# Kernel optimization log

Hardware: AMD Instinct MI355X
Metric: run time of the kernel (lower is better)

## Reference

```python
import jax, jax.numpy as jnp
import numpy as np

HIDDEN = 4096
HEADS = 64
HEAD_DIM = HIDDEN // HEADS  # 64
ROT = int(HEAD_DIM * 0.5)   # 32 rotary dims (partial rotary)
THETA = 25000.0
EPS = 1e-5
B, S = 1, 2048


def setup_inputs() -> dict:
    key = jax.random.key(0)
    ks = jax.random.split(key, 8)
    hidden_states = jax.random.normal(ks[0], (B, S, HIDDEN), dtype=jnp.float32)
    # additive causal mask: 0 on/below diagonal, -inf above
    causal = jnp.triu(jnp.full((S, S), -1e9, dtype=jnp.float32), k=1)
    attention_mask = causal[None, None, :, :]
    position_ids = jnp.arange(S, dtype=jnp.int64 if jax.config.jax_enable_x64 else jnp.int32)[None, :]
    sc = 0.02
    W_qkv = jax.random.normal(ks[1], (3 * HIDDEN, HIDDEN), dtype=jnp.float32) * sc
    b_qkv = jnp.zeros((3 * HIDDEN,), dtype=jnp.float32)
    q_ln_w = jnp.ones((HEAD_DIM,), dtype=jnp.float32)
    q_ln_b = jnp.zeros((HEAD_DIM,), dtype=jnp.float32)
    k_ln_w = jnp.ones((HEAD_DIM,), dtype=jnp.float32)
    k_ln_b = jnp.zeros((HEAD_DIM,), dtype=jnp.float32)
    W_dense = jax.random.normal(ks[2], (HIDDEN, HIDDEN), dtype=jnp.float32) * sc
    b_dense = jnp.zeros((HIDDEN,), dtype=jnp.float32)
    return dict(hidden_states=hidden_states, attention_mask=attention_mask,
                W_qkv=W_qkv, b_qkv=b_qkv, q_ln_w=q_ln_w, q_ln_b=q_ln_b,
                k_ln_w=k_ln_w, k_ln_b=k_ln_b, W_dense=W_dense, b_dense=b_dense,
                position_ids=position_ids)


def _layernorm(x, w, b):
    mu = jnp.mean(x, axis=-1, keepdims=True)
    var = jnp.var(x, axis=-1, keepdims=True)
    return (x - mu) * jax.lax.rsqrt(var + EPS) * w + b


def _rotate_half(x):
    h = x.shape[-1] // 2
    return jnp.concatenate((-x[..., h:], x[..., :h]), axis=-1)


def reference(hidden_states, attention_mask, W_qkv, b_qkv, q_ln_w, q_ln_b,
              k_ln_w, k_ln_b, W_dense, b_dense, position_ids):
    b, s, _ = hidden_states.shape
    # fused QKV projection, split interleaved per head: [b,s,H,3,d]
    fused = hidden_states @ W_qkv.T + b_qkv
    fused = fused.reshape(b, s, HEADS, 3, HEAD_DIM)
    q, k, v = fused[..., 0, :], fused[..., 1, :], fused[..., 2, :]
    # per-head QK LayerNorm (over head_dim)
    q = _layernorm(q, q_ln_w, q_ln_b)
    k = _layernorm(k, k_ln_w, k_ln_b)
    # [b,H,s,d]
    q = q.transpose(0, 2, 1, 3)
    k = k.transpose(0, 2, 1, 3)
    v = v.transpose(0, 2, 1, 3)
    # rotary embeddings (default rope, scaling 1.0)
    inv_freq = 1.0 / (THETA ** (jnp.arange(0, ROT, 2, dtype=jnp.float32) / ROT))
    freqs = position_ids.astype(jnp.float32)[:, :, None] * inv_freq[None, None, :]  # [b,s,ROT/2]
    emb = jnp.concatenate((freqs, freqs), axis=-1)  # [b,s,ROT]
    cos = jnp.cos(emb)[:, None, :, :].astype(hidden_states.dtype)  # [b,1,s,ROT]
    sin = jnp.sin(emb)[:, None, :, :].astype(hidden_states.dtype)
    # partial rotary: rotate first ROT dims, pass-through the rest
    q_rot, q_pass = q[..., :ROT], q[..., ROT:]
    k_rot, k_pass = k[..., :ROT], k[..., ROT:]
    q_rot = q_rot * cos + _rotate_half(q_rot) * sin
    k_rot = k_rot * cos + _rotate_half(k_rot) * sin
    q = jnp.concatenate((q_rot, q_pass), axis=-1)
    k = jnp.concatenate((k_rot, k_pass), axis=-1)
    # causal attention
    scores = jnp.einsum('bhqd,bhkd->bhqk', q, k) / np.sqrt(HEAD_DIM).astype(np.float32)
    scores = scores + attention_mask
    probs = jax.nn.softmax(scores.astype(jnp.float32), axis=-1).astype(q.dtype)
    attn = jnp.einsum('bhqk,bhkd->bhqd', probs, v)
    attn = attn.transpose(0, 2, 1, 3).reshape(b, s, HIDDEN)
    return attn @ W_dense.T + b_dense
```

## Files before the change

kernel.cpp:

```cpp
#include <hip/hip_runtime.h>
#include <hip/hip_bf16.h>


using short8 = __attribute__((ext_vector_type(8))) short;
using f32x4  = __attribute__((ext_vector_type(4))) float;

#define HIDDEN 4096
#define HEADS  64
#define HD     64
#define SLEN   2048
#define QSCALE 0.18033688011112042f

__device__ inline float bf2f(__hip_bfloat16 v) { return __bfloat162float(v); }
__device__ inline __hip_bfloat16 f2bf(float f) { return __float2bfloat16(f); }
__device__ inline unsigned short f2bfbits(float f) {
    return __builtin_bit_cast(unsigned short, __float2bfloat16(f));
}
__device__ inline short8 pack8(float4 a, float4 b) {
    short8 r;
    r[0] = (short)f2bfbits(a.x); r[1] = (short)f2bfbits(a.y);
    r[2] = (short)f2bfbits(a.z); r[3] = (short)f2bfbits(a.w);
    r[4] = (short)f2bfbits(b.x); r[5] = (short)f2bfbits(b.y);
    r[6] = (short)f2bfbits(b.z); r[7] = (short)f2bfbits(b.w);
    return r;
}
__device__ inline int pk2(float lo, float hi) {
    return (int)(((unsigned)f2bfbits(hi) << 16) | (unsigned)f2bfbits(lo));
}

__device__ inline void load_lds16(const void* g, void* l) {
    __builtin_amdgcn_global_load_lds(
        (const __attribute__((address_space(1))) void*)g,
        (__attribute__((address_space(3))) void*)l, 16, 0, 0);
}

__global__ __launch_bounds__(256)
void cvt_f32_bf16(const float* __restrict__ in, __hip_bfloat16* __restrict__ out, int n8)
{
    const int stride = gridDim.x * blockDim.x;
    for (int i = blockIdx.x * blockDim.x + threadIdx.x; i < n8; i += stride) {
        const float4 a = *(const float4*)(in + (size_t)i * 8);
        const float4 b = *(const float4*)(in + (size_t)i * 8 + 4);
        *(short8*)(out + (size_t)i * 8) = pack8(a, b);
    }
}

__global__ __launch_bounds__(512, 2)
void gemm_qkv(const __hip_bfloat16* __restrict__ A, const __hip_bfloat16* __restrict__ B,
              const float* __restrict__ bias,
              __hip_bfloat16* __restrict__ q0, __hip_bfloat16* __restrict__ o1,
              __hip_bfloat16* __restrict__ o2, int M, int N, int K)
{
    __shared__ __align__(16) __hip_bfloat16 Abuf[2][16384];
    __shared__ __align__(16) __hip_bfloat16 Bbuf[2][12288];

    const int tid  = threadIdx.x;
    const int wid  = tid >> 6;
    const int lane = tid & 63;
    const int lr   = lane & 15;
    const int lg   = lane >> 4;

    const int nwg = gridDim.x * gridDim.y;
    int flat = blockIdx.y * gridDim.x + blockIdx.x;
    flat = (flat & 7) * (nwg >> 3) + (flat >> 3);
    const int bm = (flat % gridDim.x) * 256;
    const int bn = (flat / gridDim.x) * 192;

    const int wr = (wid >> 2) * 128;
    const int wc = (wid & 3) * 48;

    const int scol = 8 * ((lane & 7) ^ ((lane >> 3) & 7));
    const __hip_bfloat16* PA = A + (size_t)(bm + wid * 32 + (lane >> 3)) * K + scol;
    const __hip_bfloat16* PB = B + (size_t)(bn + wid * 24 + (lane >> 3)) * K + scol;
    const int ldA = wid * 2048;
    const int ldB = wid * 1536;

#define SH_A(tile, buf) { \
    const __hip_bfloat16* g_ = PA + (size_t)(tile) * 64; \
    load_lds16(g_,                  &Abuf[buf][ldA]); \
    load_lds16(g_ + (size_t)8 * K,  &Abuf[buf][ldA + 512]); \
    load_lds16(g_ + (size_t)16 * K, &Abuf[buf][ldA + 1024]); \
    load_lds16(g_ + (size_t)24 * K, &Abuf[buf][ldA + 1536]); }
#define SH_B(tile, buf) { \
    const __hip_bfloat16* g_ = PB + (size_t)(tile) * 64; \
    load_lds16(g_,                  &Bbuf[buf][ldB]); \
    load_lds16(g_ + (size_t)8 * K,  &Bbuf[buf][ldB + 512]); \
    load_lds16(g_ + (size_t)16 * K, &Bbuf[buf][ldB + 1024]); }

    const int slot = lg ^ (lr & 7);
    const char* A0k0 = (const char*)&Abuf[0][0] + (wr + lr) * 128 + slot * 16;
    const char* A0k1 = (const char*)&Abuf[0][0] + (wr + lr) * 128 + (slot ^ 4) * 16;
    const char* A1k0 = (const char*)&Abuf[1][0] + (wr + lr) * 128 + slot * 16;
    const char* A1k1 = (const char*)&Abuf[1][0] + (wr + lr) * 128 + (slot ^ 4) * 16;
    const char* B0k0 = (const char*)&Bbuf[0][0] + (wc + lr) * 128 + slot * 16;
    const char* B0k1 = (const char*)&Bbuf[0][0] + (wc + lr) * 128 + (slot ^ 4) * 16;
    const char* B1k0 = (const char*)&Bbuf[1][0] + (wc + lr) * 128 + slot * 16;
    const char* B1k1 = (const char*)&Bbuf[1][0] + (wc + lr) * 128 + (slot ^ 4) * 16;

    f32x4 acc[8][3] = {};
    short8 af[4][2], bfL[2][2], bfH[1][2];

#define RD_AF(K0, K1, MOFF) { \
    _Pragma("unroll") \
    for (int mm = 0; mm < 4; ++mm) { \
        af[mm][0] = *(const short8*)((K0) + ((MOFF) + mm) * 2048); \
        af[mm][1] = *(const short8*)((K1) + ((MOFF) + mm) * 2048); } }
#define RD_BL(K0, K1) { \
    _Pragma("unroll") \
    for (int nn = 0; nn < 2; ++nn) { \
        bfL[nn][0] = *(const short8*)((K0) + nn * 2048); \
        bfL[nn][1] = *(const short8*)((K1) + nn * 2048); } }
#define RD_BH(K0, K1) { \
    bfH[0][0] = *(const short8*)((K0) + 2 * 2048); \
    bfH[0][1] = *(const short8*)((K1) + 2 * 2048); }
#define MFMA_BLK2(MB) \
    __builtin_amdgcn_s_setprio(1); \
    { _Pragma("unroll") \
      for (int mm = 0; mm < 4; ++mm) { \
        _Pragma("unroll") \
        for (int nn = 0; nn < 2; ++nn) { \
            acc[(MB) + mm][nn] = __builtin_amdgcn_mfma_f32_16x16x32_bf16(af[mm][0], bfL[nn][0], acc[(MB) + mm][nn], 0, 0, 0); \
            acc[(MB) + mm][nn] = __builtin_amdgcn_mfma_f32_16x16x32_bf16(af[mm][1], bfL[nn][1], acc[(MB) + mm][nn], 0, 0, 0); } } } \
    __builtin_amdgcn_s_setprio(0);
#define MFMA_BLK1(MB) \
    __builtin_amdgcn_s_setprio(1); \
    { _Pragma("unroll") \
      for (int mm = 0; mm < 4; ++mm) { \
        acc[(MB) + mm][2] = __builtin_amdgcn_mfma_f32_16x16x32_bf16(af[mm][0], bfH[0][0], acc[(MB) + mm][2], 0, 0, 0); \
        acc[(MB) + mm][2] = __builtin_amdgcn_mfma_f32_16x16x32_bf16(af[mm][1], bfH[0][1], acc[(MB) + mm][2], 0, 0, 0); } } \
    __builtin_amdgcn_s_setprio(0);

    SH_A(0, 0); SH_B(0, 0);
    SH_A(1, 1); SH_B(1, 1);
    asm volatile("s_waitcnt vmcnt(7)\n\ts_barrier" ::: "memory");

    const int nt2 = K >> 7;
    #pragma unroll 1
    for (int j = 0; j < nt2; ++j) {
        const bool st = (j < nt2 - 1);
        const int t2 = 2 * j + 2, t3 = 2 * j + 3;

        RD_AF(A0k0, A0k1, 0); RD_BL(B0k0, B0k1);
        __builtin_amdgcn_s_barrier();
        MFMA_BLK2(0);
        __builtin_amdgcn_s_barrier();

        RD_BH(B0k0, B0k1);
        __builtin_amdgcn_s_barrier();
        MFMA_BLK1(0);
        __builtin_amdgcn_s_barrier();

        RD_AF(A0k0, A0k1, 4);
        if (st) SH_B(t2, 0);
        __builtin_amdgcn_s_barrier();
        MFMA_BLK2(4);
        __builtin_amdgcn_s_barrier();

        if (st) SH_A(t2, 0);
        __builtin_amdgcn_s_barrier();
        MFMA_BLK1(4);
        if (st) asm volatile("s_waitcnt vmcnt(7)\n\ts_barrier" ::: "memory");
        else    asm volatile("s_waitcnt vmcnt(0)\n\ts_barrier" ::: "memory");

        RD_AF(A1k0, A1k1, 0); RD_BL(B1k0, B1k1);
        __builtin_amdgcn_s_barrier();
        MFMA_BLK2(0);
        __builtin_amdgcn_s_barrier();

        RD_BH(B1k0, B1k1);
        __builtin_amdgcn_s_barrier();
        MFMA_BLK1(0);
        __builtin_amdgcn_s_barrier();

        RD_AF(A1k0, A1k1, 4);
        if (st) SH_B(t3, 1);
        __builtin_amdgcn_s_barrier();
        MFMA_BLK2(4);
        __builtin_amdgcn_s_barrier();

        if (st) SH_A(t3, 1);
        __builtin_amdgcn_s_barrier();
        MFMA_BLK1(4);
        if (st) asm volatile("s_waitcnt vmcnt(7)\n\ts_barrier" ::: "memory");
    }
#undef SH_A
#undef SH_B
#undef RD_AF
#undef RD_BL
#undef RD_BH
#undef MFMA_BLK2
#undef MFMA_BLK1

    #pragma unroll
    for (int n = 0; n < 3; ++n) {
        const int cb    = bn + wc + n * 16;
        const int c64   = cb >> 6;
        const int which = c64 % 3;
        const int h     = c64 / 3;
        const int d     = (cb & 63) + lr;
        const float bb  = bias[cb + lr];

        if (which == 2) {
            #pragma unroll
            for (int m = 0; m < 8; ++m) {
                const int row = bm + wr + m * 16 + lg * 4;
                int2 w;
                w.x = pk2(acc[m][n][0] + bb, acc[m][n][1] + bb);
                w.y = pk2(acc[m][n][2] + bb, acc[m][n][3] + bb);
                *(int2*)(o2 + ((size_t)(h * HD + d)) * SLEN + row) = w;
            }
        } else {
            __hip_bfloat16* outp = (which == 0) ? q0 : o1;
            #pragma unroll
            for (int m = 0; m < 8; ++m)
                #pragma unroll
                for (int e = 0; e < 4; ++e) {
                    const int row = bm + wr + m * 16 + lg * 4 + e;
                    outp[(size_t)row * HIDDEN + h * HD + d] = f2bf(acc[m][n][e] + bb);
                }
        }
    }
}

__global__ __launch_bounds__(256, 4)
void gemm_d(const __hip_bfloat16* __restrict__ A, const __hip_bfloat16* __restrict__ B,
            const float* __restrict__ bias, float* __restrict__ C, int M, int N, int K)
{
    __shared__ __align__(16) __hip_bfloat16 Abuf[2][128 * 32];
    __shared__ __align__(16) __hip_bfloat16 Bbuf[2][128 * 32];

    const int tid  = threadIdx.x;
    const int wid  = tid >> 6;
    const int lane = tid & 63;
    const int lr   = lane & 15;
    const int lg   = lane >> 4;

    const int nwg = gridDim.x * gridDim.y;
    int flat = blockIdx.y * gridDim.x + blockIdx.x;
    flat = (flat & 7) * (nwg >> 3) + (flat >> 3);
    const int bm = (flat % gridDim.x) * 128;
    const int bn = (flat / gridDim.x) * 128;

    const int wr = (wid >> 1) * 64;
    const int wc = (wid & 1) * 64;

    const int srow = lane >> 2;
    const int sc   = lane & 3;
    const int scol = (sc ^ ((srow >> 1) & 3)) * 8;
    const __hip_bfloat16* Ag = A + (size_t)(bm + wid * 16 + srow) * K + scol;
    const __hip_bfloat16* Bg = B + (size_t)(bn + wid * 16 + srow) * K + scol;
    const int ldsW = wid * 512;

    const int rswz = (lr >> 1) & 3;
    const int rdAoff = (wr + lr) * 64 + ((lg ^ rswz) * 16);
    const int rdBoff = (wc + lr) * 64 + ((lg ^ rswz) * 16);

    f32x4 acc[4][4] = {};
    const int nt = K >> 5;

#define STG_D(t, slot) { \
    const __hip_bfloat16* gA = Ag + (size_t)(t) * 32; \
    const __hip_bfloat16* gB = Bg + (size_t)(t) * 32; \
    load_lds16(gA,                  &Abuf[slot][ldsW]); \
    load_lds16(gA + (size_t)64 * K, &Abuf[slot][ldsW + 2048]); \
    load_lds16(gB,                  &Bbuf[slot][ldsW]); \
    load_lds16(gB + (size_t)64 * K, &Bbuf[slot][ldsW + 2048]); }

    STG_D(0, 0);
    asm volatile("s_waitcnt vmcnt(0)\n\ts_barrier" ::: "memory");

    #pragma unroll 1
    for (int t = 0; t < nt; ++t) {
        const int s = t & 1;
        const char* As = (const char*)&Abuf[s][0];
        const char* Bs = (const char*)&Bbuf[s][0];

        if (t + 1 < nt) STG_D(t + 1, s ^ 1);

        short8 af[4], bf[4];
        #pragma unroll
        for (int m = 0; m < 4; ++m)
            af[m] = *(const short8*)(As + rdAoff + m * 1024);
        #pragma unroll
        for (int n = 0; n < 4; ++n)
            bf[n] = *(const short8*)(Bs + rdBoff + n * 1024);

        __builtin_amdgcn_s_setprio(1);
        #pragma unroll
        for (int m = 0; m < 4; ++m)
            #pragma unroll
            for (int n = 0; n < 4; ++n)
                acc[m][n] = __builtin_amdgcn_mfma_f32_16x16x32_bf16(af[m], bf[n], acc[m][n], 0, 0, 0);
        __builtin_amdgcn_s_setprio(0);

        asm volatile("s_waitcnt vmcnt(0)\n\ts_barrier" ::: "memory");
    }
#undef STG_D

    #pragma unroll
    for (int m = 0; m < 4; ++m)
        #pragma unroll
        for (int n = 0; n < 4; ++n) {
            const int col = bn + wc + n * 16 + lr;
            const float bv = bias[col];
            #pragma unroll
            for (int e = 0; e < 4; ++e) {
                const int row = bm + wr + m * 16 + lg * 4 + e;
                C[(size_t)row * N + col] = acc[m][n][e] + bv;
            }
        }
}

template<int MODE, bool AF32, bool BF32>
__global__ __launch_bounds__(256)
void gemm_nt(const void* __restrict__ Ap, const void* __restrict__ Bp,
             const float* __restrict__ bias,
             void* __restrict__ o0, __hip_bfloat16* __restrict__ o1,
             __hip_bfloat16* __restrict__ o2, int M, int N, int K)
{
    __shared__ __align__(16) unsigned char AbufRaw[AF32 ? 16384 : 8192];
    __shared__ __align__(16) unsigned char BbufRaw[BF32 ? 16384 : 8192];
    const int tid  = threadIdx.x;
    const int wid  = tid >> 6;
    const int lane = tid & 63;
    const int bm   = blockIdx.x * 128;
    const int bn   = blockIdx.y * 128;
    const int wr   = (wid >> 1) * 64;
    const int wc   = (wid & 1) * 64;
    const int lr   = lane & 15;
    const int lg   = lane >> 4;

    f32x4 acc[4][4] = {};

    for (int k0 = 0; k0 < K; k0 += 32) {
        __syncthreads();
        if constexpr (AF32) {
            const float* Af = (const float*)Ap;
            const int r = lane >> 3, c4 = (lane & 7) * 4;
            #pragma unroll
            for (int i = 0; i < 4; ++i) {
                const int rb = i * 32 + wid * 8;
                load_lds16(Af + (size_t)(bm + rb + r) * K + k0 + c4, (float*)AbufRaw + rb * 32);
            }
        } else {
            const __hip_bfloat16* Ab16 = (const __hip_bfloat16*)Ap;
            const int sr2 = lane >> 2, sc = (lane & 3) * 8;
            #pragma unroll
            for (int i = 0; i < 2; ++i) {
                const int rb = (wid * 2 + i) * 16;
                load_lds16(Ab16 + (size_t)(bm + rb + sr2) * K + k0 + sc,
                           (__hip_bfloat16*)AbufRaw + rb * 32);
            }
        }
        if constexpr (BF32) {
            const float* Bf = (const float*)Bp;
            const int r = lane >> 3, c4 = (lane & 7) * 4;
            #pragma unroll
            for (int i = 0; i < 4; ++i) {
                const int rb = i * 32 + wid * 8;
                load_lds16(Bf + (size_t)(bn + rb + r) * K + k0 + c4, (float*)BbufRaw + rb * 32);
            }
        } else {
            const __hip_bfloat16* Bb16 = (const __hip_bfloat16*)Bp;
            const int sr2 = lane >> 2, sc = (lane & 3) * 8;
            #pragma unroll
            for (int i = 0; i < 2; ++i) {
                const int rb = (wid * 2 + i) * 16;
                load_lds16(Bb16 + (size_t)(bn + rb + sr2) * K + k0 + sc,
                           (__hip_bfloat16*)BbufRaw + rb * 32);
            }
        }
        __syncthreads();

        short8 af[4], bfr[4];
        #pragma unroll
        for (int m = 0; m < 4; ++m) {
            const int row = wr + m * 16 + lr;
            if constexpr (AF32) {
                const float* Ab = (const float*)AbufRaw;
                af[m] = pack8(*(const float4*)(Ab + row * 32 + lg * 8),
                              *(const float4*)(Ab + row * 32 + lg * 8 + 4));
            } else {
                af[m] = *(const short8*)((const __hip_bfloat16*)AbufRaw + row * 32 + lg * 8);
            }
        }
        #pragma unroll
        for (int n = 0; n < 4; ++n) {
            const int row = wc + n * 16 + lr;
            if constexpr (BF32) {
                const float* Bb = (const float*)BbufRaw;
                bfr[n] = pack8(*(const float4*)(Bb + row * 32 + lg * 8),
                               *(const float4*)(Bb + row * 32 + lg * 8 + 4));
            } else {
                bfr[n] = *(const short8*)((const __hip_bfloat16*)BbufRaw + row * 32 + lg * 8);
            }
        }
        #pragma unroll
        for (int m = 0; m < 4; ++m)
            #pragma unroll
            for (int n = 0; n < 4; ++n)
                acc[m][n] = __builtin_amdgcn_mfma_f32_16x16x32_bf16(af[m], bfr[n], acc[m][n], 0, 0, 0);
    }

    #pragma unroll
    for (int m = 0; m < 4; ++m) {
        #pragma unroll
        for (int n = 0; n < 4; ++n) {
            const int col = bn + wc + n * 16 + lr;
            const float bv = bias[col];
            #pragma unroll
            for (int e = 0; e < 4; ++e) {
                const int row = bm + wr + m * 16 + lg * 4 + e;
                const float v = acc[m][n][e] + bv;
                if (MODE == 0) {
                    ((float*)o0)[(size_t)row * N + col] = v;
                } else {
                    const int h     = col / 192;
                    const int rem   = col - h * 192;
                    const int which = rem >> 6;
                    const int d     = rem & 63;
                    __hip_bfloat16* q0p = (__hip_bfloat16*)o0;
                    if (which == 0)      q0p[(size_t)row * HIDDEN + h * HD + d] = f2bf(v);
                    else if (which == 1) o1[(size_t)row * HIDDEN + h * HD + d] = f2bf(v);
                    else                 o2[((size_t)(h * HD + d)) * SLEN + row] = f2bf(v);
                }
            }
        }
    }
}

__global__ __launch_bounds__(256)
void ln_rope(__hip_bfloat16* __restrict__ Qp,
             __hip_bfloat16* __restrict__ Kp,
             const float* __restrict__ qw, const float* __restrict__ qb,
             const float* __restrict__ kw, const float* __restrict__ kb)
{
    const int wi   = blockIdx.x * 4 + (threadIdx.x >> 6);
    const int lane = threadIdx.x & 63;
    const int s = wi >> 6;
    const int h = wi & 63;
    const int d = lane;

    const size_t idx = (size_t)s * HIDDEN + h * HD + d;
    float q = bf2f(Qp[idx]);
    float k = bf2f(Kp[idx]);

    float qs = q, ks = k;
    #pragma unroll
    for (int m = 1; m < 64; m <<= 1) { qs += __shfl_xor(qs, m); ks += __shfl_xor(ks, m); }
    const float qmean = qs * (1.0f / 64.0f), kmean = ks * (1.0f / 64.0f);
    const float qd = q - qmean, kd = k - kmean;
    float qv = qd * qd, kv = kd * kd;
    #pragma unroll
    for (int m = 1; m < 64; m <<= 1) { qv += __shfl_xor(qv, m); kv += __shfl_xor(kv, m); }
    const float qr = rsqrtf(qv * (1.0f / 64.0f) + 1e-5f);
    const float kr = rsqrtf(kv * (1.0f / 64.0f) + 1e-5f);
    float qn = qd * qr * qw[d] + qb[d];
    float kn = kd * kr * kw[d] + kb[d];

    const float qo = __shfl_xor(qn, 16);
    const float ko = __shfl_xor(kn, 16);
    if (d < 32) {
        const int   i   = d & 15;
        const float inv = expf(-0.6329144439906461f * (float)i);
        const float ang = (float)s * inv;
        const float c = cosf(ang), sn = sinf(ang);
        const float qrh = (d < 16) ? -qo : qo;
        const float krh = (d < 16) ? -ko : ko;
        qn = qn * c + qrh * sn;
        kn = kn * c + krh * sn;
    }
    qn *= QSCALE;

    Qp[idx] = f2bf(qn);
    Kp[idx] = f2bf(kn);
}

__global__ __launch_bounds__(256)
void flash_attn(const __hip_bfloat16* __restrict__ Q,
                const __hip_bfloat16* __restrict__ Kb,
                const __hip_bfloat16* __restrict__ Vt,
                __hip_bfloat16* __restrict__ Ao)
{
    const int wid  = threadIdx.x >> 6;
    const int lane = threadIdx.x & 63;
    int bidx = blockIdx.x;
    bidx = (bidx & 7) * 64 + (bidx >> 3);
    const int qg   = 31 - (bidx & 31);
    const int h    = (bidx >> 5) * 4 + wid;
    const int lr   = lane & 15;
    const int lg   = lane >> 4;
    const int src0 = lr + (((2 * lg) & 3) << 4);
    const int src1 = src0 + 16;

    const int qrowA = (4 * qg + 0) * 16 + lr;
    const int qrowB = (4 * qg + 1) * 16 + lr;
    const int qrowC = (4 * qg + 2) * 16 + lr;
    const int qrowD = (4 * qg + 3) * 16 + lr;

    const __hip_bfloat16* qbA = Q + (size_t)qrowA * HIDDEN + h * HD + lg * 8;
    const __hip_bfloat16* qbB = Q + (size_t)qrowB * HIDDEN + h * HD + lg * 8;
    const __hip_bfloat16* qbC = Q + (size_t)qrowC * HIDDEN + h * HD + lg * 8;
    const __hip_bfloat16* qbD = Q + (size_t)qrowD * HIDDEN + h * HD + lg * 8;
    const short8 qaA0 = *(const short8*)qbA;
    const short8 qaA1 = *(const short8*)(qbA + 32);
    const short8 qaB0 = *(const short8*)qbB;
    const short8 qaB1 = *(const short8*)(qbB + 32);
    const short8 qaC0 = *(const short8*)qbC;
    const short8 qaC1 = *(const short8*)(qbC + 32);
    const short8 qaD0 = *(const short8*)qbD;
    const short8 qaD1 = *(const short8*)(qbD + 32);

    f32x4 accA[4] = {}, accB[4] = {}, accC[4] = {}, accD[4] = {};
    float lpA = 0.0f, lpB = 0.0f, lpC = 0.0f, lpD = 0.0f;

    const int nt     = 2 * qg + 2;
    const int ftiles = 2 * qg;

    const __hip_bfloat16* kp = Kb + (size_t)lr * HIDDEN + h * HD + lg * 8;
    short8 k00 = *(const short8*)kp;
    short8 k01 = *(const short8*)(kp + 32);
    short8 k10 = *(const short8*)(kp + (size_t)16 * HIDDEN);
    short8 k11 = *(const short8*)(kp + (size_t)16 * HIDDEN + 32);

#define SM_PV(MASKED, S0, S1, QROW, LP, ACC) { \
    float p0[4], p1[4]; \
    _Pragma("unroll") \
    for (int e = 0; e < 4; ++e) { \
        if (MASKED) { \
            const int krow = kv0 + lg * 4 + e; \
            p0[e] = (krow      <= (QROW)) ? exp2f(S0[e]) : 0.0f; \
            p1[e] = (krow + 16 <= (QROW)) ? exp2f(S1[e]) : 0.0f; \
        } else { \
            p0[e] = exp2f(S0[e]); \
            p1[e] = exp2f(S1[e]); \
        } \
        LP += p0[e] + p1[e]; \
    } \
    const int a0 = pk2(p0[0], p0[1]), a1 = pk2(p0[2], p0[3]); \
    const int b0 = pk2(p1[0], p1[1]), b1 = pk2(p1[2], p1[3]); \
    const int za00 = __shfl(a0, src0), za10 = __shfl(a1, src0); \
    const int za01 = __shfl(a0, src1), za11 = __shfl(a1, src1); \
    const int zb00 = __shfl(b0, src0), zb10 = __shfl(b1, src0); \
    const int zb01 = __shfl(b0, src1), zb11 = __shfl(b1, src1); \
    int4 W; \
    W.x = (lg < 2) ? za00 : zb00; \
    W.y = (lg < 2) ? za10 : zb10; \
    W.z = (lg < 2) ? za01 : zb01; \
    W.w = (lg < 2) ? za11 : zb11; \
    const short8 pB_ = __builtin_bit_cast(short8, W); \
    _Pragma("unroll") \
    for (int n = 0; n < 4; ++n) \
        ACC[n] = __builtin_amdgcn_mfma_f32_16x16x32_bf16(vf[n], pB_, ACC[n], 0, 0, 0); }

#define FA_TILE(MASKED) { \
    const int kv0 = t * 32; \
    short8 vf[4]; \
    _Pragma("unroll") \
    for (int n = 0; n < 4; ++n) \
        vf[n] = *(const short8*)(Vt + ((size_t)(h * HD + n * 16 + lr)) * SLEN + kv0 + lg * 8); \
    f32x4 sA0 = {-8.f, -8.f, -8.f, -8.f}; \
    f32x4 sA1 = {-8.f, -8.f, -8.f, -8.f}; \
    f32x4 sB0 = {-8.f, -8.f, -8.f, -8.f}; \
    f32x4 sB1 = {-8.f, -8.f, -8.f, -8.f}; \
    f32x4 sC0 = {-8.f, -8.f, -8.f, -8.f}; \
    f32x4 sC1 = {-8.f, -8.f, -8.f, -8.f}; \
    f32x4 sD0 = {-8.f, -8.f, -8.f, -8.f}; \
    f32x4 sD1 = {-8.f, -8.f, -8.f, -8.f}; \
    sA0 = __builtin_amdgcn_mfma_f32_16x16x32_bf16(k00, qaA0, sA0, 0, 0, 0); \
    sB0 = __builtin_amdgcn_mfma_f32_16x16x32_bf16(k00, qaB0, sB0, 0, 0, 0); \
    sC0 = __builtin_amdgcn_mfma_f32_16x16x32_bf16(k00, qaC0, sC0, 0, 0, 0); \
    sD0 = __builtin_amdgcn_mfma_f32_16x16x32_bf16(k00, qaD0, sD0, 0, 0, 0); \
    sA0 = __builtin_amdgcn_mfma_f32_16x16x32_bf16(k01, qaA1, sA0, 0, 0, 0); \
    sB0 = __builtin_amdgcn_mfma_f32_16x16x32_bf16(k01, qaB1, sB0, 0, 0, 0); \
    sC0 = __builtin_amdgcn_mfma_f32_16x16x32_bf16(k01, qaC1, sC0, 0, 0, 0); \
    sD0 = __builtin_amdgcn_mfma_f32_16x16x32_bf16(k01, qaD1, sD0, 0, 0, 0); \
    sA1 = __builtin_amdgcn_mfma_f32_16x16x32_bf16(k10, qaA0, sA1, 0, 0, 0); \
    sB1 = __builtin_amdgcn_mfma_f32_16x16x32_bf16(k10, qaB0, sB1, 0, 0, 0); \
    sC1 = __builtin_amdgcn_mfma_f32_16x16x32_bf16(k10, qaC0, sC1, 0, 0, 0); \
    sD1 = __builtin_amdgcn_mfma_f32_16x16x32_bf16(k10, qaD0, sD1, 0, 0, 0); \
    sA1 = __builtin_amdgcn_mfma_f32_16x16x32_bf16(k11, qaA1, sA1, 0, 0, 0); \
    sB1 = __builtin_amdgcn_mfma_f32_16x16x32_bf16(k11, qaB1, sB1, 0, 0, 0); \
    sC1 = __builtin_amdgcn_mfma_f32_16x16x32_bf16(k11, qaC1, sC1, 0, 0, 0); \
    sD1 = __builtin_amdgcn_mfma_f32_16x16x32_bf16(k11, qaD1, sD1, 0, 0, 0); \
    short8 n00, n01, n10, n11; \
    if (t + 1 < nt) { \
        const __hip_bfloat16* np = kp + (size_t)(kv0 + 32) * HIDDEN; \
        n00 = *(const short8*)np; \
        n01 = *(const short8*)(np + 32); \
        n10 = *(const short8*)(np + (size_t)16 * HIDDEN); \
        n11 = *(const short8*)(np + (size_t)16 * HIDDEN + 32); \
    } \
    SM_PV(MASKED, sA0, sA1, qrowA, lpA, accA) \
    SM_PV(MASKED, sB0, sB1, qrowB, lpB, accB) \
    SM_PV(MASKED, sC0, sC1, qrowC, lpC, accC) \
    SM_PV(MASKED, sD0, sD1, qrowD, lpD, accD) \
    k00 = n00; k01 = n01; k10 = n10; k11 = n11; }

    int t = 0;
    #pragma unroll 1
    for (; t < ftiles; ++t) FA_TILE(false)
    #pragma unroll 1
    for (; t < nt; ++t) FA_TILE(true)
#undef FA_TILE
#undef SM_PV

#define FIN(LP, INV) \
    { float lr_ = LP; lr_ += __shfl_xor(lr_, 16); lr_ += __shfl_xor(lr_, 32); INV = 1.0f / lr_; }
    float invA, invB, invC, invD;
    FIN(lpA, invA) FIN(lpB, invB) FIN(lpC, invC) FIN(lpD, invD)
#undef FIN

    __hip_bfloat16* opA = Ao + (size_t)qrowA * HIDDEN + h * HD + lg * 4;
    __hip_bfloat16* opB = Ao + (size_t)qrowB * HIDDEN + h * HD + lg * 4;
    __hip_bfloat16* opC = Ao + (size_t)qrowC * HIDDEN + h * HD + lg * 4;
    __hip_bfloat16* opD = Ao + (size_t)qrowD * HIDDEN + h * HD + lg * 4;
    #pragma unroll
    for (int n = 0; n < 4; ++n) {
        int2 w;
        w.x = pk2(accA[n][0] * invA, accA[n][1] * invA);
        w.y = pk2(accA[n][2] * invA, accA[n][3] * invA);
        *(int2*)(opA + n * 16) = w;
        w.x = pk2(accB[n][0] * invB, accB[n][1] * invB);
        w.y = pk2(accB[n][2] * invB, accB[n][3] * invB);
        *(int2*)(opB + n * 16) = w;
        w.x = pk2(accC[n][0] * invC, accC[n][1] * invC);
        w.y = pk2(accC[n][2] * invC, accC[n][3] * invC);
        *(int2*)(opC + n * 16) = w;
        w.x = pk2(accD[n][0] * invD, accD[n][1] * invD);
        w.y = pk2(accD[n][2] * invD, accD[n][3] * invD);
        *(int2*)(opD + n * 16) = w;
    }
}

extern "C" void kernel_launch(void* const* d_in, const int* in_sizes, int n_in,
                              void* d_out, int out_size, void* d_ws, size_t ws_size,
                              hipStream_t stream)
{
    const float* hidden = (const float*)d_in[0];
    const float* Wqkv = (const float*)d_in[2];
    const float* bqkv = (const float*)d_in[3];
    const float* qlw  = (const float*)d_in[4];
    const float* qlb  = (const float*)d_in[5];
    const float* klw  = (const float*)d_in[6];
    const float* klb  = (const float*)d_in[7];
    const float* Wd   = (const float*)d_in[8];
    const float* bd   = (const float*)d_in[9];

    char* ws = (char*)d_ws;
    const size_t SEG = (size_t)SLEN * HIDDEN * sizeof(__hip_bfloat16);
    if (ws_size < 4 * SEG) return;
    __hip_bfloat16* Qpre = (__hip_bfloat16*)(ws + 0 * SEG);
    __hip_bfloat16* Kpre = (__hip_bfloat16*)(ws + 1 * SEG);
    __hip_bfloat16* Vt   = (__hip_bfloat16*)(ws + 2 * SEG);
    __hip_bfloat16* Ao   = (__hip_bfloat16*)(ws + 3 * SEG);

    const bool fast = (ws_size >= 13 * SEG);

    if (fast) {
        __hip_bfloat16* hid16  = (__hip_bfloat16*)(ws + 4 * SEG);
        __hip_bfloat16* Wqkv16 = (__hip_bfloat16*)(ws + 5 * SEG);
        __hip_bfloat16* Wd16   = (__hip_bfloat16*)(ws + 11 * SEG);

        cvt_f32_bf16<<<2048, 256, 0, stream>>>(hidden, hid16,  SLEN * HIDDEN / 8);
        cvt_f32_bf16<<<2048, 256, 0, stream>>>(Wqkv,   Wqkv16, 3 * HIDDEN * HIDDEN / 8);
        cvt_f32_bf16<<<2048, 256, 0, stream>>>(Wd,     Wd16,   HIDDEN * HIDDEN / 8);

        gemm_qkv<<<dim3(8, 64), 512, 0, stream>>>(
            hid16, Wqkv16, bqkv, Qpre, Kpre, Vt, SLEN, 3 * HIDDEN, HIDDEN);
        ln_rope<<<dim3(SLEN * HEADS / 4), 256, 0, stream>>>(Qpre, Kpre, qlw, qlb, klw, klb);
        flash_attn<<<dim3((HEADS / 4) * 32), 256, 0, stream>>>(Qpre, Kpre, Vt, Ao);
        gemm_d<<<dim3(16, 32), 256, 0, stream>>>(
            Ao, Wd16, bd, (float*)d_out, SLEN, HIDDEN, HIDDEN);
    } else {
        gemm_nt<1, true, true><<<dim3(16, 96), 256, 0, stream>>>(
            hidden, Wqkv, bqkv, Qpre, Kpre, Vt, SLEN, 3 * HIDDEN, HIDDEN);
        ln_rope<<<dim3(SLEN * HEADS / 4), 256, 0, stream>>>(Qpre, Kpre, qlw, qlb, klw, klb);
        flash_attn<<<dim3((HEADS / 4) * 32), 256, 0, stream>>>(Qpre, Kpre, Vt, Ao);
        gemm_nt<0, false, true><<<dim3(16, 32), 256, 0, stream>>>(
            Ao, Wd, bd, d_out, nullptr, nullptr, SLEN, HIDDEN, HIDDEN);
    }
}
```

Measured before the change: 529.8 us.

## Overlap dense-weight conversion with flash attention and merge input conversions

The hidden and QKV-weight fp32-to-bf16 conversions are merged into one launch. The dense-weight conversion moves into extra blocks of the flash attention kernel so it runs alongside the attention blocks instead of as a separate launch. This removes two kernel launches and should hide the W_dense conversion's memory traffic behind the compute-bound attention. The extra blocks compete with attention blocks for CU slots and bandwidth, which could slow attention's tail.

```diff
diff --git a/kernel.cpp b/kernel.cpp
--- a/kernel.cpp
+++ b/kernel.cpp
@@ -10,6 +10,7 @@
 #define HD     64
 #define SLEN   2048
 #define QSCALE 0.18033688011112042f
+#define FLASH_BLOCKS 512
 
 __device__ inline float bf2f(__hip_bfloat16 v) { return __bfloat162float(v); }
 __device__ inline __hip_bfloat16 f2bf(float f) { return __float2bfloat16(f); }
@@ -42,6 +43,26 @@
         const float4 a = *(const float4*)(in + (size_t)i * 8);
         const float4 b = *(const float4*)(in + (size_t)i * 8 + 4);
         *(short8*)(out + (size_t)i * 8) = pack8(a, b);
+    }
+}
+
+__global__ __launch_bounds__(256)
+void cvt2_f32_bf16(const float* __restrict__ ia, __hip_bfloat16* __restrict__ oa, int na8,
+                   const float* __restrict__ ib, __hip_bfloat16* __restrict__ ob, int nb8)
+{
+    const int stride = gridDim.x * blockDim.x;
+    const int total  = na8 + nb8;
+    for (int i = blockIdx.x * blockDim.x + threadIdx.x; i < total; i += stride) {
+        if (i < na8) {
+            const float4 a = *(const float4*)(ia + (size_t)i * 8);
+            const float4 b = *(const float4*)(ia + (size_t)i * 8 + 4);
+            *(short8*)(oa + (size_t)i * 8) = pack8(a, b);
+        } else {
+            const int j = i - na8;
+            const float4 a = *(const float4*)(ib + (size_t)j * 8);
+            const float4 b = *(const float4*)(ib + (size_t)j * 8 + 4);
+            *(short8*)(ob + (size_t)j * 8) = pack8(a, b);
+        }
     }
 }
 
@@ -480,10 +501,26 @@
 void flash_attn(const __hip_bfloat16* __restrict__ Q,
                 const __hip_bfloat16* __restrict__ Kb,
                 const __hip_bfloat16* __restrict__ Vt,
-                __hip_bfloat16* __restrict__ Ao)
+                __hip_bfloat16* __restrict__ Ao,
+                const float* __restrict__ WdF,
+                __hip_bfloat16* __restrict__ Wd16,
+                int cvtBlocks)
 {
     const int wid  = threadIdx.x >> 6;
     const int lane = threadIdx.x & 63;
+
+    if (blockIdx.x >= FLASH_BLOCKS) {
+        if (WdF == nullptr) return;
+        const int n8     = HIDDEN * HIDDEN / 8;
+        const int stride = cvtBlocks * 256;
+        for (int i = (blockIdx.x - FLASH_BLOCKS) * 256 + threadIdx.x; i < n8; i += stride) {
+            const float4 a = *(const float4*)(WdF + (size_t)i * 8);
+            const float4 b = *(const float4*)(WdF + (size_t)i * 8 + 4);
+            *(short8*)(Wd16 + (size_t)i * 8) = pack8(a, b);
+        }
+        return;
+    }
+
     int bidx = blockIdx.x;
     bidx = (bidx & 7) * 64 + (bidx >> 3);
     const int qg   = 31 - (bidx & 31);
@@ -662,21 +699,23 @@
         __hip_bfloat16* Wqkv16 = (__hip_bfloat16*)(ws + 5 * SEG);
         __hip_bfloat16* Wd16   = (__hip_bfloat16*)(ws + 11 * SEG);
 
-        cvt_f32_bf16<<<2048, 256, 0, stream>>>(hidden, hid16,  SLEN * HIDDEN / 8);
-        cvt_f32_bf16<<<2048, 256, 0, stream>>>(Wqkv,   Wqkv16, 3 * HIDDEN * HIDDEN / 8);
-        cvt_f32_bf16<<<2048, 256, 0, stream>>>(Wd,     Wd16,   HIDDEN * HIDDEN / 8);
+        cvt2_f32_bf16<<<2048, 256, 0, stream>>>(
+            hidden, hid16, SLEN * HIDDEN / 8,
+            Wqkv, Wqkv16, 3 * HIDDEN * HIDDEN / 8);
 
         gemm_qkv<<<dim3(8, 64), 512, 0, stream>>>(
             hid16, Wqkv16, bqkv, Qpre, Kpre, Vt, SLEN, 3 * HIDDEN, HIDDEN);
         ln_rope<<<dim3(SLEN * HEADS / 4), 256, 0, stream>>>(Qpre, Kpre, qlw, qlb, klw, klb);
-        flash_attn<<<dim3((HEADS / 4) * 32), 256, 0, stream>>>(Qpre, Kpre, Vt, Ao);
+        flash_attn<<<dim3(FLASH_BLOCKS + 512), 256, 0, stream>>>(
+            Qpre, Kpre, Vt, Ao, Wd, Wd16, 512);
         gemm_d<<<dim3(16, 32), 256, 0, stream>>>(
             Ao, Wd16, bd, (float*)d_out, SLEN, HIDDEN, HIDDEN);
     } else {
         gemm_nt<1, true, true><<<dim3(16, 96), 256, 0, stream>>>(
             hidden, Wqkv, bqkv, Qpre, Kpre, Vt, SLEN, 3 * HIDDEN, HIDDEN);
         ln_rope<<<dim3(SLEN * HEADS / 4), 256, 0, stream>>>(Qpre, Kpre, qlw, qlb, klw, klb);
-        flash_attn<<<dim3((HEADS / 4) * 32), 256, 0, stream>>>(Qpre, Kpre, Vt, Ao);
+        flash_attn<<<dim3(FLASH_BLOCKS), 256, 0, stream>>>(
+            Qpre, Kpre, Vt, Ao, nullptr, nullptr, 0);
         gemm_nt<0, false, true><<<dim3(16, 32), 256, 0, stream>>>(
             Ao, Wd, bd, d_out, nullptr, nullptr, SLEN, HIDDEN, HIDDEN);
     }
```

New measurement: 534.4 us. About the same (+0.9%).
